# Kernel optimization log

Measured on AMD Instinct MI355X. Metric: run time of the kernel, lower is better.

Reference implementation:

```python
import jax, jax.numpy as jnp
import numpy as np

N_NODES = 50000
N_EDGES = 800000
IN, HID, OUT = 128, [128, 128], 64


def setup_inputs() -> dict:
    key = jax.random.key(0)
    ks = jax.random.split(key, 10)
    inp = {
        'in_feat': jax.random.normal(ks[0], (N_NODES, IN), dtype=jnp.float32),
        'src': jax.random.randint(ks[1], (N_EDGES,), 0, N_NODES, dtype=jnp.int32),
        'dst': jax.random.randint(ks[2], (N_EDGES,), 0, N_NODES, dtype=jnp.int32),
    }
    dims = [IN] + HID + [OUT]  # [128,128,128,64]
    for i in range(3):
        fan_in = dims[i]
        inp[f'W{i}'] = jax.random.normal(ks[3 + i], (dims[i + 1], dims[i]), dtype=jnp.float32) / np.sqrt(fan_in)
        inp[f'b{i}'] = jnp.zeros((dims[i + 1],), dtype=jnp.float32)
    return inp


def _sage_gcn_layer(x, W, b, src, dst, n_nodes):
    # DGL SAGEConv aggregator_type='gcn':
    #   neigh = segment_sum of src feats over dst edges (graph already has self-loops)
    #   h = (neigh + x) / (in_degree + 1); out = h @ W.T + b
    msg = x[src]                                             # [E, d] gather
    neigh = jax.ops.segment_sum(msg, dst, num_segments=n_nodes)
    deg = jax.ops.segment_sum(jnp.ones(src.shape[0], x.dtype), dst, num_segments=n_nodes)
    h = (neigh + x) / (deg[:, None] + 1.0)
    return h @ W.T + b


def reference(in_feat, src, dst, W0, b0, W1, b1, W2, b2):
    n = in_feat.shape[0]
    # remove_self_loop + add_self_loop -> exactly one self loop per node
    loop = jnp.arange(n, dtype=src.dtype)
    src_f = jnp.concatenate([src, loop])
    dst_f = jnp.concatenate([dst, loop])
    # Dropout(0.5) is identity in eval mode.
    h = in_feat
    h = jax.nn.relu(_sage_gcn_layer(h, W0, b0, src_f, dst_f, n))
    h = jax.nn.relu(_sage_gcn_layer(h, W1, b1, src_f, dst_f, n))
    h = _sage_gcn_layer(h, W2, b2, src_f, dst_f, n)
    return h
```

## Files before the change

### kernel.cpp

```cpp
#include <hip/hip_runtime.h>
#include <hip/hip_bf16.h>


#define NFEAT 128
#define BKT_CAP 12288
#define CHUNK 64

using bf16x8 = __attribute__((ext_vector_type(8))) short;
using f32x4  = __attribute__((ext_vector_type(4))) float;

__device__ __forceinline__ ushort f2bf(float f) {
    unsigned u = __float_as_uint(f);
    u = (u + 0x7fffu + ((u >> 16) & 1u)) >> 16;
    return (ushort)u;
}
__device__ __forceinline__ float bflo(unsigned v) { return __uint_as_float(v << 16); }
__device__ __forceinline__ float bfhi(unsigned v) { return __uint_as_float(v & 0xffff0000u); }

__device__ __forceinline__ int xcc_id() {
    int x;
    asm volatile("s_getreg_b32 %0, hwreg(HW_REG_XCC_ID)" : "=s"(x));
    return x & 7;
}


__global__ __launch_bounds__(256) void k_init(unsigned* __restrict__ esrc_u32, int fillN, unsigned sent2,
                                              int* __restrict__ ctl, ushort* __restrict__ Ybuf, int n) {
    int i = blockIdx.x * 256 + threadIdx.x;
    if (i < fillN) {
        esrc_u32[i] = sent2;
    } else if (i < fillN + 320) {
        ctl[i - fillN] = 0;
    } else if (i < fillN + 320 + 64) {
        int j = i - fillN - 320;
        int p = j >> 4, k = j & 15;
        ((unsigned*)(Ybuf + (size_t)p * (n + 1) * 32 + (size_t)n * 32))[k] = 0u;
    }
}


__global__ __launch_bounds__(256) void k_bin(const int* __restrict__ src, const int* __restrict__ dst,
                                             int* __restrict__ gcur, unsigned* __restrict__ pairs, int ne) {
    __shared__ int lcnt[128];
    __shared__ int lbase[128];
    int tid = threadIdx.x;
    if (tid < 128) lcnt[tid] = 0;
    __syncthreads();
    int e0 = blockIdx.x * 4096;
    int myrank[16];
    int mybkt[16];
    unsigned mypair[16];
    #pragma unroll
    for (int i = 0; i < 16; ++i) {
        int e = e0 + tid + i * 256;
        if (e < ne) {
            int s = src[e], d = dst[e];
            int b = d >> 9;
            mybkt[i]  = b;
            mypair[i] = (unsigned)(s & 0xffff) | ((unsigned)(d & 511) << 16);
            myrank[i] = atomicAdd(&lcnt[b], 1);
        } else mybkt[i] = -1;
    }
    __syncthreads();
    if (tid < 128) lbase[tid] = lcnt[tid] ? atomicAdd(&gcur[tid], lcnt[tid]) : 0;
    __syncthreads();
    #pragma unroll
    for (int i = 0; i < 16; ++i) {
        if (mybkt[i] >= 0) {
            int pos = lbase[mybkt[i]] + myrank[i];
            if (pos < BKT_CAP) pairs[(size_t)mybkt[i] * BKT_CAP + pos] = mypair[i];
        }
    }
}

__global__ __launch_bounds__(256) void k_cnt(const unsigned* __restrict__ pairs, const int* __restrict__ gcur,
                                             int* __restrict__ cnt, int n) {
    __shared__ int lcnt[512];
    int b = blockIdx.x, tid = threadIdx.x;
    for (int i = tid; i < 512; i += 256) lcnt[i] = 0;
    __syncthreads();
    int m = gcur[b];
    if (m > BKT_CAP) m = BKT_CAP;
    const unsigned* p = pairs + (size_t)b * BKT_CAP;
    for (int i = tid; i < m; i += 256) atomicAdd(&lcnt[p[i] >> 16], 1);
    __syncthreads();
    int base = b * 512;
    for (int i = tid; i < 512; i += 256) {
        int node = base + i;
        if (node < n) cnt[node] = lcnt[i];
    }
}

__global__ __launch_bounds__(1024) void k_prep_win(const int* __restrict__ cnt, int* __restrict__ perm,
                                                   int* __restrict__ part, int* __restrict__ tots, int n) {
    __shared__ int hist[256];
    __shared__ int hcur[256];
    __shared__ int wtot[16];
    __shared__ int wpre[16];
    int tid  = threadIdx.x;
    int lane = tid & 63;
    int wv   = tid >> 6;
    int base = blockIdx.x * 1024;
    if (tid < 256) hist[tid] = 0;
    __syncthreads();
    int i = base + tid;
    bool act = i < n;
    int c = 0, d = 0, rank = 0;
    if (act) {
        c = cnt[i];
        d = c > 255 ? 255 : c;
        rank = atomicAdd(&hist[d], 1);
    }
    __syncthreads();
    {
        int v = (tid < 256) ? hist[tid] : 0;
        int val = v;
        #pragma unroll
        for (int off = 1; off < 64; off <<= 1) {
            int t = __shfl_up(val, off);
            if (lane >= off) val += t;
        }
        if (lane == 63) wtot[wv] = val;
        __syncthreads();
        if (tid == 0) {
            int s = 0;
            #pragma unroll
            for (int w = 0; w < 4; ++w) { wpre[w] = s; s += wtot[w]; }
        }
        __syncthreads();
        if (tid < 256) hcur[tid] = val - v + wpre[wv];
        __syncthreads();
        if (act) perm[base + hcur[d] + rank] = i;
        __syncthreads();
    }
    {
        int p = act ? ((c + 7) & ~7) : 0;
        int val = p;
        #pragma unroll
        for (int off = 1; off < 64; off <<= 1) {
            int t = __shfl_up(val, off);
            if (lane >= off) val += t;
        }
        if (lane == 63) wtot[wv] = val;
        __syncthreads();
        if (tid == 0) {
            int s = 0;
            #pragma unroll
            for (int w = 0; w < 16; ++w) { wpre[w] = s; s += wtot[w]; }
            tots[blockIdx.x] = s;
        }
        __syncthreads();
        if (act) part[i] = val - p + wpre[wv];
    }
}

__global__ __launch_bounds__(1024) void k_scan_tops(int* __restrict__ tots, int* __restrict__ total_out, int nch) {
    __shared__ int wtot[16];
    __shared__ int wpre[16];
    int tid  = threadIdx.x;
    int lane = tid & 63;
    int wv   = tid >> 6;
    int v    = (tid < nch) ? tots[tid] : 0;
    int val  = v;
    #pragma unroll
    for (int off = 1; off < 64; off <<= 1) {
        int t = __shfl_up(val, off);
        if (lane >= off) val += t;
    }
    if (lane == 63) wtot[wv] = val;
    __syncthreads();
    if (tid == 0) {
        int s = 0;
        #pragma unroll
        for (int w = 0; w < 16; ++w) { wpre[w] = s; s += wtot[w]; }
        *total_out = s;
    }
    __syncthreads();
    int excl = val - v + wpre[wv];
    if (tid < nch) tots[tid] = excl;
}

__global__ __launch_bounds__(1024) void k_scan_add(int* __restrict__ offs, const int* __restrict__ tots, int n) {
    int i = blockIdx.x * 1024 + threadIdx.x;
    if (i < n) offs[i] += tots[blockIdx.x];
}

__global__ __launch_bounds__(256) void k_scatter(const unsigned* __restrict__ pairs, const int* __restrict__ gcur,
                                                 const int* __restrict__ offs, ushort* __restrict__ esrc, int n) {
    __shared__ int lcur[512];
    __shared__ int loffs[512];
    int b = blockIdx.x, tid = threadIdx.x;
    int base = b * 512;
    for (int i = tid; i < 512; i += 256) {
        lcur[i] = 0;
        int node = base + i;
        loffs[i] = (node < n) ? offs[node] : 0;
    }
    __syncthreads();
    int m = gcur[b];
    if (m > BKT_CAP) m = BKT_CAP;
    const unsigned* p = pairs + (size_t)b * BKT_CAP;
    for (int i = tid; i < m; i += 256) {
        unsigned pr = p[i];
        int dlow = pr >> 16;
        int r = atomicAdd(&lcur[dlow], 1);
        esrc[loffs[dlow] + r] = (ushort)(pr & 0xffffu);
    }
}


__global__ __launch_bounds__(256) void k_cast3(const float* __restrict__ a, int na,
                                               const float* __restrict__ b, int nb,
                                               const float* __restrict__ c, int nc,
                                               ushort* __restrict__ out) {
    int i = blockIdx.x * 256 + threadIdx.x;
    if (i >= na + nb + nc) return;
    float v = (i < na) ? a[i] : ((i < na + nb) ? b[i - na] : c[i - na - nb]);
    out[i] = f2bf(v);
}


template <typename InT, int N, bool PLANES_IN>
__global__ __launch_bounds__(256) void k_gemm_mfma(const InT* __restrict__ X, const ushort* __restrict__ Wb,
                                                   ushort* __restrict__ Y, int M, int Mp) {
    int w    = threadIdx.x >> 6;
    int lane = threadIdx.x & 63;
    int rowf = blockIdx.x * 64 + w * 16 + (lane & 15);
    int kb   = (lane >> 4) * 8;

    bf16x8 a[4];
    if (rowf < M) {
        #pragma unroll
        for (int ks = 0; ks < 4; ++ks) {
            if constexpr (PLANES_IN) {
                a[ks] = *(const bf16x8*)((const ushort*)X + (size_t)ks * Mp * 32 + (size_t)rowf * 32 + kb);
            } else {
                const float* xp = (const float*)X + (size_t)rowf * 128 + ks * 32 + kb;
                float4 f0 = *(const float4*)xp;
                float4 f1 = *(const float4*)(xp + 4);
                bf16x8 t;
                t[0] = f2bf(f0.x); t[1] = f2bf(f0.y); t[2] = f2bf(f0.z); t[3] = f2bf(f0.w);
                t[4] = f2bf(f1.x); t[5] = f2bf(f1.y); t[6] = f2bf(f1.z); t[7] = f2bf(f1.w);
                a[ks] = t;
            }
        }
    } else {
        #pragma unroll
        for (int ks = 0; ks < 4; ++ks) {
            bf16x8 z = {0, 0, 0, 0, 0, 0, 0, 0};
            a[ks] = z;
        }
    }

    constexpr int NT = N / 16;
    f32x4 acc[NT];
    #pragma unroll
    for (int nt = 0; nt < NT; ++nt) acc[nt] = (f32x4){0.f, 0.f, 0.f, 0.f};

    #pragma unroll
    for (int nt = 0; nt < NT; ++nt) {
        const ushort* wp = Wb + (size_t)(nt * 16 + (lane & 15)) * 128 + kb;
        #pragma unroll
        for (int ks = 0; ks < 4; ++ks) {
            bf16x8 b = *(const bf16x8*)(wp + ks * 32);
            acc[nt] = __builtin_amdgcn_mfma_f32_16x16x32_bf16(a[ks], b, acc[nt], 0, 0, 0);
        }
    }

    int c  = lane & 15;
    int r0 = blockIdx.x * 64 + w * 16 + (lane >> 4) * 4;
    #pragma unroll
    for (int j = 0; j < 4; ++j) {
        int r = r0 + j;
        if (r < M) {
            #pragma unroll
            for (int nt = 0; nt < NT; ++nt)
                Y[(size_t)(nt >> 1) * Mp * 32 + (size_t)r * 32 + (nt & 1) * 16 + c] = (ushort)f2bf(acc[nt][j]);
        }
    }
}


#define ACC8(T)  { a0 += bflo((T).x); a1 += bfhi((T).x); a2 += bflo((T).y); a3 += bfhi((T).y); \
                   a4 += bflo((T).z); a5 += bfhi((T).z); a6 += bflo((T).w); a7 += bfhi((T).w); }

template <bool RELU>
__global__ __launch_bounds__(256) void k_agg128(const ushort* __restrict__ Yp, const int* __restrict__ offs,
                                                const int* __restrict__ cnt, const ushort* __restrict__ esrc,
                                                const float* __restrict__ bias, ushort* __restrict__ Zp,
                                                const int* __restrict__ perm, int* __restrict__ qh,
                                                int n, int nchunk) {
    __shared__ int sQ, sT;
    if (threadIdx.x == 0) {
        int pref = xcc_id() & 3;
        int t = -1, qsel = 0;
        #pragma unroll
        for (int a = 0; a < 4; ++a) {
            int cand = (pref + a) & 3;
            int tt = atomicAdd(&qh[cand * 16], 1);
            if (tt < nchunk) { qsel = cand; t = tt; break; }
        }
        sQ = qsel; sT = t;
    }
    __syncthreads();
    int q = sQ, t = sT;
    if (t < 0) return;
    int lane = threadIdx.x & 63;
    int wv   = threadIdx.x >> 6;
    int g    = lane >> 2;
    int sub  = lane & 3;
    int idx  = t * CHUNK + wv * 16 + g;
    bool active = idx < n;
    int nd = 0, start = 0, deg = 0;
    if (active) {
        nd    = perm[idx];
        start = offs[nd];
        deg   = cnt[nd];
    }
    const uint4* Y4 = (const uint4*)(Yp + (size_t)q * (n + 1) * 32);
    uint4*       Z4 = (uint4*)(Zp + (size_t)q * (n + 1) * 32);

    float a0 = 0.f, a1 = 0.f, a2 = 0.f, a3 = 0.f, a4 = 0.f, a5 = 0.f, a6 = 0.f, a7 = 0.f;

    int nblk = active ? ((deg + 7) >> 3) : 0;
    const uint4* ep = (const uint4*)(esrc + start);
    uint4 ib = ep[0];
    #pragma unroll 2
    for (int b = 0; b < nblk; ++b) {
        uint4 ibn = ep[b + 1];
        unsigned s0 = ib.x & 0xffffu, s1 = ib.x >> 16;
        unsigned s2 = ib.y & 0xffffu, s3 = ib.y >> 16;
        unsigned s4 = ib.z & 0xffffu, s5 = ib.z >> 16;
        unsigned s6 = ib.w & 0xffffu, s7 = ib.w >> 16;
        uint4 t0 = Y4[(size_t)s0 * 4 + sub];
        uint4 t1 = Y4[(size_t)s1 * 4 + sub];
        uint4 t2 = Y4[(size_t)s2 * 4 + sub];
        uint4 t3 = Y4[(size_t)s3 * 4 + sub];
        uint4 t4 = Y4[(size_t)s4 * 4 + sub];
        uint4 t5 = Y4[(size_t)s5 * 4 + sub];
        uint4 t6 = Y4[(size_t)s6 * 4 + sub];
        uint4 t7 = Y4[(size_t)s7 * 4 + sub];
        ACC8(t0); ACC8(t1); ACC8(t2); ACC8(t3); ACC8(t4); ACC8(t5); ACC8(t6); ACC8(t7);
        ib = ibn;
    }

    if (active) {
        float scale = 1.0f / (float)(deg + 2);
        uint4 sf = Y4[(size_t)nd * 4 + sub];
        int f0 = q * 32 + sub * 8;
        float4 bA = *(const float4*)&bias[f0];
        float4 bB = *(const float4*)&bias[f0 + 4];
        float r0 = (a0 + 2.f * bflo(sf.x)) * scale + bA.x;
        float r1 = (a1 + 2.f * bfhi(sf.x)) * scale + bA.y;
        float r2 = (a2 + 2.f * bflo(sf.y)) * scale + bA.z;
        float r3 = (a3 + 2.f * bfhi(sf.y)) * scale + bA.w;
        float r4 = (a4 + 2.f * bflo(sf.z)) * scale + bB.x;
        float r5 = (a5 + 2.f * bfhi(sf.z)) * scale + bB.y;
        float r6 = (a6 + 2.f * bflo(sf.w)) * scale + bB.z;
        float r7 = (a7 + 2.f * bfhi(sf.w)) * scale + bB.w;
        if (RELU) {
            r0 = fmaxf(r0, 0.f); r1 = fmaxf(r1, 0.f); r2 = fmaxf(r2, 0.f); r3 = fmaxf(r3, 0.f);
            r4 = fmaxf(r4, 0.f); r5 = fmaxf(r5, 0.f); r6 = fmaxf(r6, 0.f); r7 = fmaxf(r7, 0.f);
        }
        uint4 o;
        o.x = (unsigned)f2bf(r0) | ((unsigned)f2bf(r1) << 16);
        o.y = (unsigned)f2bf(r2) | ((unsigned)f2bf(r3) << 16);
        o.z = (unsigned)f2bf(r4) | ((unsigned)f2bf(r5) << 16);
        o.w = (unsigned)f2bf(r6) | ((unsigned)f2bf(r7) << 16);
        Z4[(size_t)nd * 4 + sub] = o;
    }
}

__global__ __launch_bounds__(256) void k_agg64(const ushort* __restrict__ Yp, const int* __restrict__ offs,
                                               const int* __restrict__ cnt, const ushort* __restrict__ esrc,
                                               const float* __restrict__ bias, float* __restrict__ Z,
                                               const int* __restrict__ perm, int* __restrict__ qh,
                                               int n, int nchunk) {
    __shared__ int sQ, sT;
    if (threadIdx.x == 0) {
        int pref = xcc_id() & 1;
        int t = -1, qsel = 0;
        #pragma unroll
        for (int a = 0; a < 2; ++a) {
            int cand = (pref + a) & 1;
            int tt = atomicAdd(&qh[cand * 16], 1);
            if (tt < nchunk) { qsel = cand; t = tt; break; }
        }
        sQ = qsel; sT = t;
    }
    __syncthreads();
    int h = sQ, t = sT;
    if (t < 0) return;
    int lane = threadIdx.x & 63;
    int wv   = threadIdx.x >> 6;
    int g    = lane >> 2;
    int sub  = lane & 3;
    int idx  = t * CHUNK + wv * 16 + g;
    bool active = idx < n;
    int nd = 0, start = 0, deg = 0;
    if (active) {
        nd    = perm[idx];
        start = offs[nd];
        deg   = cnt[nd];
    }
    const uint4* Y4 = (const uint4*)(Yp + (size_t)h * (n + 1) * 32);

    float a0 = 0.f, a1 = 0.f, a2 = 0.f, a3 = 0.f, a4 = 0.f, a5 = 0.f, a6 = 0.f, a7 = 0.f;

    int nblk = active ? ((deg + 7) >> 3) : 0;
    const uint4* ep = (const uint4*)(esrc + start);
    uint4 ib = ep[0];
    #pragma unroll 2
    for (int b = 0; b < nblk; ++b) {
        uint4 ibn = ep[b + 1];
        unsigned s0 = ib.x & 0xffffu, s1 = ib.x >> 16;
        unsigned s2 = ib.y & 0xffffu, s3 = ib.y >> 16;
        unsigned s4 = ib.z & 0xffffu, s5 = ib.z >> 16;
        unsigned s6 = ib.w & 0xffffu, s7 = ib.w >> 16;
        uint4 t0 = Y4[(size_t)s0 * 4 + sub];
        uint4 t1 = Y4[(size_t)s1 * 4 + sub];
        uint4 t2 = Y4[(size_t)s2 * 4 + sub];
        uint4 t3 = Y4[(size_t)s3 * 4 + sub];
        uint4 t4 = Y4[(size_t)s4 * 4 + sub];
        uint4 t5 = Y4[(size_t)s5 * 4 + sub];
        uint4 t6 = Y4[(size_t)s6 * 4 + sub];
        uint4 t7 = Y4[(size_t)s7 * 4 + sub];
        ACC8(t0); ACC8(t1); ACC8(t2); ACC8(t3); ACC8(t4); ACC8(t5); ACC8(t6); ACC8(t7);
        ib = ibn;
    }

    if (active) {
        float scale = 1.0f / (float)(deg + 2);
        uint4 sf = Y4[(size_t)nd * 4 + sub];
        int f0 = h * 32 + sub * 8;
        float4 bA = *(const float4*)&bias[f0];
        float4 bB = *(const float4*)&bias[f0 + 4];
        float4 oA, oB;
        oA.x = (a0 + 2.f * bflo(sf.x)) * scale + bA.x;
        oA.y = (a1 + 2.f * bfhi(sf.x)) * scale + bA.y;
        oA.z = (a2 + 2.f * bflo(sf.y)) * scale + bA.z;
        oA.w = (a3 + 2.f * bfhi(sf.y)) * scale + bA.w;
        oB.x = (a4 + 2.f * bflo(sf.z)) * scale + bB.x;
        oB.y = (a5 + 2.f * bfhi(sf.z)) * scale + bB.y;
        oB.z = (a6 + 2.f * bflo(sf.w)) * scale + bB.z;
        oB.w = (a7 + 2.f * bfhi(sf.w)) * scale + bB.w;
        float* zr = Z + (size_t)nd * 64 + f0;
        *(float4*)zr       = oA;
        *(float4*)(zr + 4) = oB;
    }
}


extern "C" void kernel_launch(void* const* d_in, const int* in_sizes, int n_in,
                              void* d_out, int out_size, void* d_ws, size_t ws_size,
                              hipStream_t stream) {
    const float* in_feat = (const float*)d_in[0];
    const int*   src     = (const int*)d_in[1];
    const int*   dst     = (const int*)d_in[2];
    const float* W0      = (const float*)d_in[3];
    const float* b0      = (const float*)d_in[4];
    const float* W1      = (const float*)d_in[5];
    const float* b1      = (const float*)d_in[6];
    const float* W2      = (const float*)d_in[7];
    const float* b2      = (const float*)d_in[8];
    float* out = (float*)d_out;

    const int n  = in_sizes[0] / NFEAT;
    const int ne = in_sizes[1];
    const int nch = (n + 1023) / 1024;
    const int NB  = (n + 511) >> 9;
    const int nchunk = (n + CHUNK - 1) / CHUNK;
    const int escap = (ne + 8 * n + 31) & ~15;

    int* offs       = (int*)d_ws;
    int* tots       = offs + (((n + 1) + 3) & ~3);
    int* gcur       = tots + 1024;
    int* qh         = gcur + 128;
    int* cnt        = qh + 192;
    int* perm       = cnt + ((n + 3) & ~3);
    unsigned* pairs = (unsigned*)(perm + ((n + 3) & ~3));
    ushort* esrc    = (ushort*)(pairs + (size_t)128 * BKT_CAP);
    ushort* Wb      = esrc + escap;
    ushort* Ybuf    = Wb + 40960;
    ushort* Zbuf    = Ybuf + (size_t)(n + 1) * NFEAT;

    const int fillN = escap / 2;
    const unsigned sent2 = ((unsigned)n << 16) | (unsigned)n;
    k_init<<<(fillN + 320 + 64 + 255) / 256, 256, 0, stream>>>((unsigned*)esrc, fillN, sent2, gcur, Ybuf, n);

    k_bin<<<(ne + 4095) / 4096, 256, 0, stream>>>(src, dst, gcur, pairs, ne);
    k_cnt<<<NB, 256, 0, stream>>>(pairs, gcur, cnt, n);
    k_prep_win<<<nch, 1024, 0, stream>>>(cnt, perm, offs, tots, n);
    k_scan_tops<<<1, 1024, 0, stream>>>(tots, offs + n, nch);
    k_scan_add<<<nch, 1024, 0, stream>>>(offs, tots, n);
    k_scatter<<<NB, 256, 0, stream>>>(pairs, gcur, offs, esrc, n);

    k_cast3<<<(40960 + 255) / 256, 256, 0, stream>>>(W0, 16384, W1, 16384, W2, 8192, Wb);
    const ushort* Wb0 = Wb;
    const ushort* Wb1 = Wb + 16384;
    const ushort* Wb2 = Wb + 32768;

    const int gg = (n + 63) / 64;
    const int Mp = n + 1;

    k_gemm_mfma<float, 128, false><<<gg, 256, 0, stream>>>(in_feat, Wb0, Ybuf, n, Mp);
    k_agg128<true><<<4 * nchunk, 256, 0, stream>>>(Ybuf, offs, cnt, esrc, b0, Zbuf, perm, qh, n, nchunk);
    k_gemm_mfma<ushort, 128, true><<<gg, 256, 0, stream>>>(Zbuf, Wb1, Ybuf, n, Mp);
    k_agg128<true><<<4 * nchunk, 256, 0, stream>>>(Ybuf, offs, cnt, esrc, b1, Zbuf, perm, qh + 64, n, nchunk);
    k_gemm_mfma<ushort, 64, true><<<gg, 256, 0, stream>>>(Zbuf, Wb2, Ybuf, n, Mp);
    k_agg64<<<2 * nchunk, 256, 0, stream>>>(Ybuf, offs, cnt, esrc, b2, out, perm, qh + 128, n, nchunk);

    (void)ws_size; (void)n_in; (void)out_size;
}
```

Baseline: 221.2 us.

## Fuse graph-prep kernels, fold weight cast into init, double GEMM rows per block

The per-node count, degree histogram and offset scan are merged into a single kernel. A global atomic replaces the separate block-total scan and add passes, so each block now claims an arbitrary but disjoint range of offsets. The weight fp32-to-bf16 cast moves into the init kernel, which removes another launch. The MFMA GEMM now handles 128 rows per block with two accumulator sets, reusing each weight fragment twice at the cost of more registers. Offsets no longer follow node order across blocks, and the total is no longer written at offs[n].

Measured after the change: 200.0 us. 9.6% less time.

```diff
diff --git a/kernel.cpp b/kernel.cpp
--- a/kernel.cpp
+++ b/kernel.cpp
@@ -25,16 +25,22 @@
 
 
 __global__ __launch_bounds__(256) void k_init(unsigned* __restrict__ esrc_u32, int fillN, unsigned sent2,
-                                              int* __restrict__ ctl, ushort* __restrict__ Ybuf, int n) {
+                                              int* __restrict__ ctl, ushort* __restrict__ Ybuf, int n,
+                                              const float* __restrict__ W0, const float* __restrict__ W1,
+                                              const float* __restrict__ W2, ushort* __restrict__ Wb) {
     int i = blockIdx.x * 256 + threadIdx.x;
     if (i < fillN) {
         esrc_u32[i] = sent2;
-    } else if (i < fillN + 320) {
+    } else if (i < fillN + 336) {
         ctl[i - fillN] = 0;
-    } else if (i < fillN + 320 + 64) {
-        int j = i - fillN - 320;
+    } else if (i < fillN + 336 + 64) {
+        int j = i - fillN - 336;
         int p = j >> 4, k = j & 15;
         ((unsigned*)(Ybuf + (size_t)p * (n + 1) * 32 + (size_t)n * 32))[k] = 0u;
+    } else if (i < fillN + 336 + 64 + 40960) {
+        int j = i - fillN - 336 - 64;
+        float v = (j < 16384) ? W0[j] : ((j < 32768) ? W1[j - 16384] : W2[j - 32768]);
+        Wb[j] = f2bf(v);
     }
 }
 
@@ -73,44 +79,40 @@
     }
 }
 
-__global__ __launch_bounds__(256) void k_cnt(const unsigned* __restrict__ pairs, const int* __restrict__ gcur,
-                                             int* __restrict__ cnt, int n) {
-    __shared__ int lcnt[512];
-    int b = blockIdx.x, tid = threadIdx.x;
-    for (int i = tid; i < 512; i += 256) lcnt[i] = 0;
-    __syncthreads();
-    int m = gcur[b];
-    if (m > BKT_CAP) m = BKT_CAP;
-    const unsigned* p = pairs + (size_t)b * BKT_CAP;
-    for (int i = tid; i < m; i += 256) atomicAdd(&lcnt[p[i] >> 16], 1);
-    __syncthreads();
-    int base = b * 512;
-    for (int i = tid; i < 512; i += 256) {
-        int node = base + i;
-        if (node < n) cnt[node] = lcnt[i];
-    }
-}
-
-__global__ __launch_bounds__(1024) void k_prep_win(const int* __restrict__ cnt, int* __restrict__ perm,
-                                                   int* __restrict__ part, int* __restrict__ tots, int n) {
+
+__global__ __launch_bounds__(1024) void k_cntprep(const unsigned* __restrict__ pairs, const int* __restrict__ gcur,
+                                                  int* __restrict__ cnt, int* __restrict__ perm,
+                                                  int* __restrict__ offs, int* __restrict__ gbase, int n) {
+    __shared__ int lcnt[1024];
     __shared__ int hist[256];
     __shared__ int hcur[256];
     __shared__ int wtot[16];
     __shared__ int wpre[16];
+    __shared__ int sbase;
     int tid  = threadIdx.x;
     int lane = tid & 63;
     int wv   = tid >> 6;
     int base = blockIdx.x * 1024;
+    lcnt[tid] = 0;
     if (tid < 256) hist[tid] = 0;
     __syncthreads();
-    int i = base + tid;
+    #pragma unroll
+    for (int h = 0; h < 2; ++h) {
+        int bkt = blockIdx.x * 2 + h;
+        int m = gcur[bkt];
+        if (m > BKT_CAP) m = BKT_CAP;
+        const unsigned* p = pairs + (size_t)bkt * BKT_CAP;
+        for (int i = tid; i < m; i += 1024)
+            atomicAdd(&lcnt[(int)(p[i] >> 16) + h * 512], 1);
+    }
+    __syncthreads();
+    int i   = base + tid;
     bool act = i < n;
-    int c = 0, d = 0, rank = 0;
-    if (act) {
-        c = cnt[i];
-        d = c > 255 ? 255 : c;
-        rank = atomicAdd(&hist[d], 1);
-    }
+    int c = act ? lcnt[tid] : 0;
+    if (act) cnt[i] = c;
+    int d = c > 255 ? 255 : c;
+    int rank = 0;
+    if (act) rank = atomicAdd(&hist[d], 1);
     __syncthreads();
     {
         int v = (tid < 256) ? hist[tid] : 0;
@@ -134,8 +136,8 @@
         __syncthreads();
     }
     {
-        int p = act ? ((c + 7) & ~7) : 0;
-        int val = p;
+        int p8 = act ? ((c + 7) & ~7) : 0;
+        int val = p8;
         #pragma unroll
         for (int off = 1; off < 64; off <<= 1) {
             int t = __shfl_up(val, off);
@@ -147,43 +149,13 @@
             int s = 0;
             #pragma unroll
             for (int w = 0; w < 16; ++w) { wpre[w] = s; s += wtot[w]; }
-            tots[blockIdx.x] = s;
-        }
-        __syncthreads();
-        if (act) part[i] = val - p + wpre[wv];
-    }
-}
-
-__global__ __launch_bounds__(1024) void k_scan_tops(int* __restrict__ tots, int* __restrict__ total_out, int nch) {
-    __shared__ int wtot[16];
-    __shared__ int wpre[16];
-    int tid  = threadIdx.x;
-    int lane = tid & 63;
-    int wv   = tid >> 6;
-    int v    = (tid < nch) ? tots[tid] : 0;
-    int val  = v;
-    #pragma unroll
-    for (int off = 1; off < 64; off <<= 1) {
-        int t = __shfl_up(val, off);
-        if (lane >= off) val += t;
-    }
-    if (lane == 63) wtot[wv] = val;
-    __syncthreads();
-    if (tid == 0) {
-        int s = 0;
-        #pragma unroll
-        for (int w = 0; w < 16; ++w) { wpre[w] = s; s += wtot[w]; }
-        *total_out = s;
-    }
-    __syncthreads();
-    int excl = val - v + wpre[wv];
-    if (tid < nch) tots[tid] = excl;
-}
-
-__global__ __launch_bounds__(1024) void k_scan_add(int* __restrict__ offs, const int* __restrict__ tots, int n) {
-    int i = blockIdx.x * 1024 + threadIdx.x;
-    if (i < n) offs[i] += tots[blockIdx.x];
-}
+            sbase = atomicAdd(gbase, s);
+        }
+        __syncthreads();
+        if (act) offs[i] = sbase + val - p8 + wpre[wv];
+    }
+}
+
 
 __global__ __launch_bounds__(256) void k_scatter(const unsigned* __restrict__ pairs, const int* __restrict__ gcur,
                                                  const int* __restrict__ offs, ushort* __restrict__ esrc, int n) {
@@ -209,53 +181,50 @@
 }
 
 
-__global__ __launch_bounds__(256) void k_cast3(const float* __restrict__ a, int na,
-                                               const float* __restrict__ b, int nb,
-                                               const float* __restrict__ c, int nc,
-                                               ushort* __restrict__ out) {
-    int i = blockIdx.x * 256 + threadIdx.x;
-    if (i >= na + nb + nc) return;
-    float v = (i < na) ? a[i] : ((i < na + nb) ? b[i - na] : c[i - na - nb]);
-    out[i] = f2bf(v);
-}
-
-
 template <typename InT, int N, bool PLANES_IN>
 __global__ __launch_bounds__(256) void k_gemm_mfma(const InT* __restrict__ X, const ushort* __restrict__ Wb,
                                                    ushort* __restrict__ Y, int M, int Mp) {
     int w    = threadIdx.x >> 6;
     int lane = threadIdx.x & 63;
-    int rowf = blockIdx.x * 64 + w * 16 + (lane & 15);
     int kb   = (lane >> 4) * 8;
-
-    bf16x8 a[4];
-    if (rowf < M) {
-        #pragma unroll
-        for (int ks = 0; ks < 4; ++ks) {
-            if constexpr (PLANES_IN) {
-                a[ks] = *(const bf16x8*)((const ushort*)X + (size_t)ks * Mp * 32 + (size_t)rowf * 32 + kb);
-            } else {
-                const float* xp = (const float*)X + (size_t)rowf * 128 + ks * 32 + kb;
-                float4 f0 = *(const float4*)xp;
-                float4 f1 = *(const float4*)(xp + 4);
-                bf16x8 t;
-                t[0] = f2bf(f0.x); t[1] = f2bf(f0.y); t[2] = f2bf(f0.z); t[3] = f2bf(f0.w);
-                t[4] = f2bf(f1.x); t[5] = f2bf(f1.y); t[6] = f2bf(f1.z); t[7] = f2bf(f1.w);
-                a[ks] = t;
+    int rbase = blockIdx.x * 128 + w * 16 + (lane & 15);
+
+    bf16x8 a0[4], a1[4];
+    #pragma unroll
+    for (int set = 0; set < 2; ++set) {
+        int rowf = rbase + set * 64;
+        bf16x8* a = set ? a1 : a0;
+        if (rowf < M) {
+            #pragma unroll
+            for (int ks = 0; ks < 4; ++ks) {
+                if constexpr (PLANES_IN) {
+                    a[ks] = *(const bf16x8*)((const ushort*)X + (size_t)ks * Mp * 32 + (size_t)rowf * 32 + kb);
+                } else {
+                    const float* xp = (const float*)X + (size_t)rowf * 128 + ks * 32 + kb;
+                    float4 f0 = *(const float4*)xp;
+                    float4 f1 = *(const float4*)(xp + 4);
+                    bf16x8 t;
+                    t[0] = f2bf(f0.x); t[1] = f2bf(f0.y); t[2] = f2bf(f0.z); t[3] = f2bf(f0.w);
+                    t[4] = f2bf(f1.x); t[5] = f2bf(f1.y); t[6] = f2bf(f1.z); t[7] = f2bf(f1.w);
+                    a[ks] = t;
+                }
             }
-        }
-    } else {
-        #pragma unroll
-        for (int ks = 0; ks < 4; ++ks) {
-            bf16x8 z = {0, 0, 0, 0, 0, 0, 0, 0};
-            a[ks] = z;
+        } else {
+            #pragma unroll
+            for (int ks = 0; ks < 4; ++ks) {
+                bf16x8 z = {0, 0, 0, 0, 0, 0, 0, 0};
+                a[ks] = z;
+            }
         }
     }
 
     constexpr int NT = N / 16;
-    f32x4 acc[NT];
-    #pragma unroll
-    for (int nt = 0; nt < NT; ++nt) acc[nt] = (f32x4){0.f, 0.f, 0.f, 0.f};
+    f32x4 acc0[NT], acc1[NT];
+    #pragma unroll
+    for (int nt = 0; nt < NT; ++nt) {
+        acc0[nt] = (f32x4){0.f, 0.f, 0.f, 0.f};
+        acc1[nt] = (f32x4){0.f, 0.f, 0.f, 0.f};
+    }
 
     #pragma unroll
     for (int nt = 0; nt < NT; ++nt) {
@@ -263,19 +232,24 @@
         #pragma unroll
         for (int ks = 0; ks < 4; ++ks) {
             bf16x8 b = *(const bf16x8*)(wp + ks * 32);
-            acc[nt] = __builtin_amdgcn_mfma_f32_16x16x32_bf16(a[ks], b, acc[nt], 0, 0, 0);
+            acc0[nt] = __builtin_amdgcn_mfma_f32_16x16x32_bf16(a0[ks], b, acc0[nt], 0, 0, 0);
+            acc1[nt] = __builtin_amdgcn_mfma_f32_16x16x32_bf16(a1[ks], b, acc1[nt], 0, 0, 0);
         }
     }
 
     int c  = lane & 15;
-    int r0 = blockIdx.x * 64 + w * 16 + (lane >> 4) * 4;
-    #pragma unroll
-    for (int j = 0; j < 4; ++j) {
-        int r = r0 + j;
-        if (r < M) {
-            #pragma unroll
-            for (int nt = 0; nt < NT; ++nt)
-                Y[(size_t)(nt >> 1) * Mp * 32 + (size_t)r * 32 + (nt & 1) * 16 + c] = (ushort)f2bf(acc[nt][j]);
+    int rr = blockIdx.x * 128 + w * 16 + (lane >> 4) * 4;
+    #pragma unroll
+    for (int set = 0; set < 2; ++set) {
+        f32x4* acc = set ? acc1 : acc0;
+        #pragma unroll
+        for (int j = 0; j < 4; ++j) {
+            int r = rr + set * 64 + j;
+            if (r < M) {
+                #pragma unroll
+                for (int nt = 0; nt < NT; ++nt)
+                    Y[(size_t)(nt >> 1) * Mp * 32 + (size_t)r * 32 + (nt & 1) * 16 + c] = (ushort)f2bf(acc[nt][j]);
+            }
         }
     }
 }
@@ -473,10 +447,10 @@
     const int escap = (ne + 8 * n + 31) & ~15;
 
     int* offs       = (int*)d_ws;
-    int* tots       = offs + (((n + 1) + 3) & ~3);
-    int* gcur       = tots + 1024;
+    int* gcur       = offs + ((n + 4) & ~3);
     int* qh         = gcur + 128;
-    int* cnt        = qh + 192;
+    int* gbase      = qh + 192;
+    int* cnt        = gbase + 16;
     int* perm       = cnt + ((n + 3) & ~3);
     unsigned* pairs = (unsigned*)(perm + ((n + 3) & ~3));
     ushort* esrc    = (ushort*)(pairs + (size_t)128 * BKT_CAP);
@@ -486,21 +460,19 @@
 
     const int fillN = escap / 2;
     const unsigned sent2 = ((unsigned)n << 16) | (unsigned)n;
-    k_init<<<(fillN + 320 + 64 + 255) / 256, 256, 0, stream>>>((unsigned*)esrc, fillN, sent2, gcur, Ybuf, n);
+    const int initN = fillN + 336 + 64 + 40960;
+    k_init<<<(initN + 255) / 256, 256, 0, stream>>>((unsigned*)esrc, fillN, sent2, gcur, Ybuf, n,
+                                                    W0, W1, W2, Wb);
 
     k_bin<<<(ne + 4095) / 4096, 256, 0, stream>>>(src, dst, gcur, pairs, ne);
-    k_cnt<<<NB, 256, 0, stream>>>(pairs, gcur, cnt, n);
-    k_prep_win<<<nch, 1024, 0, stream>>>(cnt, perm, offs, tots, n);
-    k_scan_tops<<<1, 1024, 0, stream>>>(tots, offs + n, nch);
-    k_scan_add<<<nch, 1024, 0, stream>>>(offs, tots, n);
+    k_cntprep<<<nch, 1024, 0, stream>>>(pairs, gcur, cnt, perm, offs, gbase, n);
     k_scatter<<<NB, 256, 0, stream>>>(pairs, gcur, offs, esrc, n);
 
-    k_cast3<<<(40960 + 255) / 256, 256, 0, stream>>>(W0, 16384, W1, 16384, W2, 8192, Wb);
     const ushort* Wb0 = Wb;
     const ushort* Wb1 = Wb + 16384;
     const ushort* Wb2 = Wb + 32768;
 
-    const int gg = (n + 63) / 64;
+    const int gg = (n + 127) / 128;
     const int Mp = n + 1;
 
     k_gemm_mfma<float, 128, false><<<gg, 256, 0, stream>>>(in_feat, Wb0, Ybuf, n, Mp);
```
